# Kernel optimization log

Measured on AMD Instinct MI355X. Metric: run time of the kernel, lower is better.

## Reference

```python
import jax, jax.numpy as jnp
import numpy as np
import math

B, S, HID = 1, 2048, 2048
NH, NKV, HD = 32, 8, 64
GROUPS = NH // NKV
BOOST_SCALE, NARROW_SCALE = 1.0, 4.0
NEG = -1e9


def rope_cos_sin(seq_len, scale):
    inv_freq = 1.0 / (10000.0 ** (jnp.arange(0, HD, 2, dtype=jnp.float32) / HD))
    t = jnp.arange(seq_len, dtype=jnp.float32) / scale
    freqs = jnp.outer(t, inv_freq)                      # [s, hd/2]
    emb = jnp.concatenate([freqs, freqs], axis=-1)      # [s, hd]
    return jnp.cos(emb), jnp.sin(emb)


def rotate_half(x):
    x1, x2 = x[..., : HD // 2], x[..., HD // 2:]
    return jnp.concatenate([-x2, x1], axis=-1)


def apply_rope(q, k, cos, sin, position_ids):
    c = cos[position_ids][:, None]                      # [b,1,s,hd]
    s = sin[position_ids][:, None]
    return q * c + rotate_half(q) * s, k * c + rotate_half(k) * s


def setup_inputs() -> dict:
    key = jax.random.key(0)
    ks = jax.random.split(key, 5)
    hidden_states = jax.random.normal(ks[0], (B, S, HID), dtype=jnp.float32)
    i = jnp.arange(S)[:, None]
    j = jnp.arange(S)[None, :]
    attention_mask = jnp.where(j <= i, 0.0, NEG).astype(jnp.float32)[None, None]  # [1,1,S,S]
    position_ids = jnp.broadcast_to(jnp.arange(S, dtype=jnp.int32)[None], (B, S))
    sc = 1.0 / math.sqrt(HID)
    Wq = jax.random.normal(ks[1], (NH * HD, HID), dtype=jnp.float32) * sc
    Wk = jax.random.normal(ks[2], (NKV * HD, HID), dtype=jnp.float32) * sc
    Wv = jax.random.normal(ks[3], (NKV * HD, HID), dtype=jnp.float32) * sc
    Wo = jax.random.normal(ks[4], (HID, HID), dtype=jnp.float32) * sc
    return dict(hidden_states=hidden_states, attention_mask=attention_mask,
                position_ids=position_ids, Wq=Wq, Wk=Wk, Wv=Wv, Wo=Wo)


def reference(hidden_states, attention_mask, position_ids, Wq, Wk, Wv, Wo):
    b, q_len, _ = hidden_states.shape
    kv_seq_len = q_len

    q = (hidden_states @ Wq.T).reshape(b, q_len, NH, HD).transpose(0, 2, 1, 3)   # [b,H,s,hd]
    k = (hidden_states @ Wk.T).reshape(b, q_len, NKV, HD).transpose(0, 2, 1, 3)  # [b,Hkv,s,hd]
    v = (hidden_states @ Wv.T).reshape(b, q_len, NKV, HD).transpose(0, 2, 1, 3)

    boost_cos, boost_sin = rope_cos_sin(kv_seq_len, BOOST_SCALE)
    narrow_cos, narrow_sin = rope_cos_sin(kv_seq_len + 30, NARROW_SCALE)
    bq, bk = apply_rope(q, k, boost_cos, boost_sin, position_ids)
    nq, nk = apply_rope(q, k, narrow_cos, narrow_sin, position_ids)

    # repeat_kv (GQA)
    bk = jnp.repeat(bk, GROUPS, axis=1)
    nk = jnp.repeat(nk, GROUPS, axis=1)
    v = jnp.repeat(v, GROUPS, axis=1)

    inv_sqrt = 1.0 / math.sqrt(HD)
    big = jnp.einsum('bhqd,bhkd->bhqk', bq, bk) * inv_sqrt
    small = jnp.einsum('bhqd,bhkd->bhqk', nq, nk) * inv_sqrt
    big = big + attention_mask
    small = small + attention_mask

    # neighbor mask: tril minus (for rows >= context_length) tril(diag=context_length)
    # which zeroes those rows entirely -> neighbor = (j <= i) & (i < context_length)
    context_length = q_len - 10
    i = jnp.arange(q_len)[:, None]
    j = jnp.arange(kv_seq_len)[None, :]
    neighbor = (j <= i) & (i < context_length)

    merged = jnp.where(neighbor, big, small)
    probs = jax.nn.softmax(merged.astype(jnp.float32), axis=-1).astype(q.dtype)
    attn = jnp.einsum('bhqk,bhkd->bhqd', probs, v)
    attn = attn.transpose(0, 2, 1, 3).reshape(b, q_len, HID)
    return attn @ Wo.T
```

## Files before the change

kernel.cpp:

```cpp
#include <hip/hip_runtime.h>
#include <math.h>

#define S_LEN 2048
#define HIDN  2048
#define NH    32
#define NKV   8
#define HD    64
#define KVW   (NKV * HD)
#define CTX   (S_LEN - 10)
#define MASKV (-30000.0f)

typedef unsigned short u16;
typedef __attribute__((ext_vector_type(4))) float f32x4;
typedef __attribute__((ext_vector_type(8))) short s16x8;

__device__ __forceinline__ float bf2f(u16 u) {
  union { unsigned int i; float f; } v; v.i = ((unsigned int)u) << 16; return v.f;
}
__device__ __forceinline__ u16 f2bf(float f) {
  union { float f; unsigned int i; } v; v.f = f;
  unsigned int r = v.i + 0x7fffu + ((v.i >> 16) & 1u);
  return (u16)(r >> 16);
}

__global__ __launch_bounds__(256) void conv_all(
    const float* __restrict__ h,  const float* __restrict__ wq,
    const float* __restrict__ wk, const float* __restrict__ wv,
    const float* __restrict__ wo,
    u16* __restrict__ Hb, u16* __restrict__ Wqb, u16* __restrict__ Wkb,
    u16* __restrict__ Wvb, u16* __restrict__ Wob)
{
  const int i = blockIdx.x * 256 + threadIdx.x;
  const float* src; u16* dst; int off;
  if      (i < 1048576) { src = h;  dst = Hb;  off = i; }
  else if (i < 2097152) { src = wq; dst = Wqb; off = i - 1048576; }
  else if (i < 2359296) { src = wk; dst = Wkb; off = i - 2097152; }
  else if (i < 2621440) { src = wv; dst = Wvb; off = i - 2359296; }
  else                  { src = wo; dst = Wob; off = i - 2621440; }
  const float4 f4 = ((const float4*)src)[off];
  ushort4 o4;
  o4.x = f2bf(f4.x); o4.y = f2bf(f4.y); o4.z = f2bf(f4.z); o4.w = f2bf(f4.w);
  ((ushort4*)dst)[off] = o4;
}

#define BM 128
#define BN 128
#define BK 64

template<int OF32>
__device__ __forceinline__ void gemm_body(
    u16* __restrict__ As, u16* __restrict__ Bs,
    const u16* __restrict__ A, const u16* __restrict__ B, void* __restrict__ Cv,
    int N, int K, int row0, int col0, int otrans)
{
  const int tid  = threadIdx.x;
  const int wave = tid >> 6;
  const int lane = tid & 63;
  const int wr = (wave >> 1) * 64;
  const int wc = (wave & 1) * 64;

  f32x4 acc[4][4] = {};

  const int srow = wave * 8 + (lane >> 3);
  const int scol = (lane & 7) * 8;

  for (int kt = 0; kt < K; kt += BK) {
#pragma unroll
    for (int it = 0; it < 4; ++it) {
      const u16* gA = A + (size_t)(row0 + it * 32 + srow) * K + kt + scol;
      const u16* gB = B + (size_t)(col0 + it * 32 + srow) * K + kt + scol;
      u16* lA = &As[(it * 32 + wave * 8) * BK];
      u16* lB = &Bs[(it * 32 + wave * 8) * BK];
      __builtin_amdgcn_global_load_lds((const __attribute__((address_space(1))) void*)gA,
                                       (__attribute__((address_space(3))) void*)lA, 16, 0, 0);
      __builtin_amdgcn_global_load_lds((const __attribute__((address_space(1))) void*)gB,
                                       (__attribute__((address_space(3))) void*)lB, 16, 0, 0);
    }
    __syncthreads();
#pragma unroll
    for (int kk = 0; kk < 2; ++kk) {
      const int ko = kk * 32 + (lane >> 4) * 8;
      s16x8 af[4], bg[4];
#pragma unroll
      for (int mi = 0; mi < 4; ++mi)
        af[mi] = *(const s16x8*)&As[(wr + mi * 16 + (lane & 15)) * BK + ko];
#pragma unroll
      for (int ni = 0; ni < 4; ++ni)
        bg[ni] = *(const s16x8*)&Bs[(wc + ni * 16 + (lane & 15)) * BK + ko];
#pragma unroll
      for (int mi = 0; mi < 4; ++mi)
#pragma unroll
        for (int ni = 0; ni < 4; ++ni)
          acc[mi][ni] = __builtin_amdgcn_mfma_f32_16x16x32_bf16(af[mi], bg[ni], acc[mi][ni], 0, 0, 0);
    }
    __syncthreads();
  }

  const int rq = (lane >> 4) * 4;
  const int cq = lane & 15;
#pragma unroll
  for (int mi = 0; mi < 4; ++mi)
#pragma unroll
    for (int ni = 0; ni < 4; ++ni) {
      const int r = row0 + wr + mi * 16 + rq;
      const int c = col0 + wc + ni * 16 + cq;
      if (otrans) {
        ushort4 o4;
        o4.x = f2bf(acc[mi][ni][0]); o4.y = f2bf(acc[mi][ni][1]);
        o4.z = f2bf(acc[mi][ni][2]); o4.w = f2bf(acc[mi][ni][3]);
        *(ushort4*)&((u16*)Cv)[(size_t)c * S_LEN + r] = o4;
      } else {
#pragma unroll
        for (int t = 0; t < 4; ++t) {
          if (OF32) ((float*)Cv)[(size_t)(r + t) * N + c] = acc[mi][ni][t];
          else      ((u16*)Cv)[(size_t)(r + t) * N + c]   = f2bf(acc[mi][ni][t]);
        }
      }
    }
}

__global__ __launch_bounds__(256) void gemm_qkv(
    const u16* __restrict__ A, const u16* __restrict__ Wq, const u16* __restrict__ Wk,
    const u16* __restrict__ Wv, u16* __restrict__ Q, u16* __restrict__ Kb, u16* __restrict__ Vt)
{
  __shared__ u16 As[BM * BK];
  __shared__ u16 Bs[BN * BK];
  const int bn = blockIdx.x;
  const int row0 = blockIdx.y * BM;
  const u16* Bp; u16* Cp; int N; int col0; int ot;
  if (bn < 16)      { Bp = Wq; Cp = Q;  N = HIDN; col0 = bn * BN;        ot = 0; }
  else if (bn < 20) { Bp = Wk; Cp = Kb; N = KVW;  col0 = (bn - 16) * BN; ot = 0; }
  else              { Bp = Wv; Cp = Vt; N = KVW;  col0 = (bn - 20) * BN; ot = 1; }
  gemm_body<0>(As, Bs, A, Bp, Cp, N, HIDN, row0, col0, ot);
}

__global__ __launch_bounds__(256) void gemm_out(
    const u16* __restrict__ A, const u16* __restrict__ B, float* __restrict__ C, int N, int K)
{
  __shared__ u16 As[BM * BK];
  __shared__ u16 Bs[BN * BK];
  gemm_body<1>(As, Bs, A, B, C, N, K, blockIdx.y * BM, blockIdx.x * BN, 0);
}

__global__ __launch_bounds__(256) void rope_kernel(
    u16* __restrict__ Q, u16* __restrict__ Kb, u16* __restrict__ Kn,
    const int* __restrict__ pos_ids)
{
  const int idx = blockIdx.x * 256 + threadIdx.x;
  const int totq = S_LEN * NH * (HD / 2);
  const float LN1E4 = 9.210340371976184f;
  if (idx < totq) {
    const int d = idx & 31;
    const int h = (idx >> 5) & (NH - 1);
    const int i = idx >> 10;
    const float f = expf(-(float)(2 * d) * (1.0f / HD) * LN1E4);
    const int pos = pos_ids[i];
    const float scl = (i < CTX) ? 1.0f : 0.25f;
    const float ang = ((float)pos * scl) * f;
    const float c = cosf(ang), s = sinf(ang);
    u16* p = Q + (size_t)i * HIDN + h * HD + d;
    const float x1 = bf2f(p[0]), x2 = bf2f(p[32]);
    p[0]  = f2bf((x1 * c - x2 * s) * 0.125f);
    p[32] = f2bf((x2 * c + x1 * s) * 0.125f);
  } else {
    const int k = idx - totq;
    if (k >= S_LEN * NKV * (HD / 2)) return;
    const int d  = k & 31;
    const int kh = (k >> 5) & (NKV - 1);
    const int j  = k >> 8;
    const float f = expf(-(float)(2 * d) * (1.0f / HD) * LN1E4);
    const float pos = (float)pos_ids[j];
    const float cb = cosf(pos * f),          sb = sinf(pos * f);
    const float cn = cosf(pos * 0.25f * f),  sn = sinf(pos * 0.25f * f);
    const size_t off = (size_t)j * KVW + kh * HD + d;
    u16* pb = Kb + off;
    u16* pn = Kn + off;
    const float x1 = bf2f(pb[0]), x2 = bf2f(pb[32]);
    pn[0]  = f2bf(x1 * cn - x2 * sn);
    pn[32] = f2bf(x2 * cn + x1 * sn);
    pb[0]  = f2bf(x1 * cb - x2 * sb);
    pb[32] = f2bf(x2 * cb + x1 * sb);
  }
}

#define PAD 8
__global__ __launch_bounds__(256) void attn_mfma(
    const u16* __restrict__ Q, const u16* __restrict__ K, const u16* __restrict__ Kn,
    const u16* __restrict__ Vt, u16* __restrict__ O)
{
  __shared__ __align__(16) u16 Ks[64][HD + PAD];
  __shared__ __align__(16) u16 Kns[64][HD + PAD];
  __shared__ __align__(16) u16 Vts[HD][64 + PAD];
  __shared__ __align__(16) u16 Ps[4][16][64 + PAD];

  const int tid  = threadIdx.x;
  const int wave = tid >> 6;
  const int lane = tid & 63;
  const int l15  = lane & 15;
  const int quad = lane >> 4;
  const int h    = blockIdx.y;
  const int kh   = h >> 2;
  const int pr   = blockIdx.x;

  int sa[4], sb[4];
#pragma unroll
  for (int it = 0; it < 4; ++it) {
    const int u = it * 256 + tid;
    sa[it] = u >> 4;
    sb[it] = (u & 15) * 4;
  }

  for (int phase = 0; phase < 2; ++phase) {
    const int qt = phase ? pr : 31 - pr;
    const int i_base = qt * 64;
    const int rw0 = i_base + wave * 16;
    const bool mixed_blk = (qt == 31);
    const bool mixed_wv  = mixed_blk && (rw0 + 15 >= CTX);

    s16x8 aq[2];
#pragma unroll
    for (int ks = 0; ks < 2; ++ks)
      aq[ks] = *(const s16x8*)(Q + (size_t)(rw0 + l15) * HIDN + h * HD + ks * 32 + quad * 8);

    f32x4 acc_o[4] = {};
    float l_[4] = {0.f, 0.f, 0.f, 0.f};

    const int ntiles = qt + 1;
    ushort4 kr[4], vr[4], knr[4];
#pragma unroll
    for (int it = 0; it < 4; ++it) {
      kr[it] = *(const ushort4*)(K  + (size_t)(0 + sa[it]) * KVW + kh * HD + sb[it]);
      vr[it] = *(const ushort4*)(Vt + (size_t)(kh * HD + sa[it]) * S_LEN + 0 + sb[it]);
      if (mixed_blk) knr[it] = *(const ushort4*)(Kn + (size_t)(0 + sa[it]) * KVW + kh * HD + sb[it]);
    }

    for (int t = 0; t < ntiles; ++t) {
      const int jt = t * 64;
      __syncthreads();
#pragma unroll
      for (int it = 0; it < 4; ++it) {
        *(ushort4*)&Ks[sa[it]][sb[it]]  = kr[it];
        *(ushort4*)&Vts[sa[it]][sb[it]] = vr[it];
        if (mixed_blk) *(ushort4*)&Kns[sa[it]][sb[it]] = knr[it];
      }
      __syncthreads();
      if (t + 1 < ntiles) {
        const int jn = jt + 64;
#pragma unroll
        for (int it = 0; it < 4; ++it) {
          kr[it] = *(const ushort4*)(K  + (size_t)(jn + sa[it]) * KVW + kh * HD + sb[it]);
          vr[it] = *(const ushort4*)(Vt + (size_t)(kh * HD + sa[it]) * S_LEN + jn + sb[it]);
          if (mixed_blk) knr[it] = *(const ushort4*)(Kn + (size_t)(jn + sa[it]) * KVW + kh * HD + sb[it]);
        }
      }

      f32x4 sc4[4] = {};
#pragma unroll
      for (int ks = 0; ks < 2; ++ks) {
        const int ko = ks * 32 + quad * 8;
#pragma unroll
        for (int nb = 0; nb < 4; ++nb) {
          const s16x8 bk = *(const s16x8*)&Ks[nb * 16 + l15][ko];
          sc4[nb] = __builtin_amdgcn_mfma_f32_16x16x32_bf16(aq[ks], bk, sc4[nb], 0, 0, 0);
        }
      }
      if (mixed_wv) {
        f32x4 sc4n[4] = {};
#pragma unroll
        for (int ks = 0; ks < 2; ++ks) {
          const int ko = ks * 32 + quad * 8;
#pragma unroll
          for (int nb = 0; nb < 4; ++nb) {
            const s16x8 bk = *(const s16x8*)&Kns[nb * 16 + l15][ko];
            sc4n[nb] = __builtin_amdgcn_mfma_f32_16x16x32_bf16(aq[ks], bk, sc4n[nb], 0, 0, 0);
          }
        }
#pragma unroll
        for (int reg = 0; reg < 4; ++reg) {
          const bool narrow = (rw0 + quad * 4 + reg >= CTX);
#pragma unroll
          for (int nb = 0; nb < 4; ++nb)
            sc4[nb][reg] = narrow ? sc4n[nb][reg] : sc4[nb][reg];
        }
      }

      const int lr0 = quad * 4;
#pragma unroll
      for (int reg = 0; reg < 4; ++reg) {
        const int rowg = rw0 + lr0 + reg;
#pragma unroll
        for (int nb = 0; nb < 4; ++nb) {
          float p = __expf(fminf(sc4[nb][reg], 60.f));
          p = (jt + nb * 16 + l15 > rowg) ? 0.f : p;
          l_[reg] += p;
          Ps[wave][lr0 + reg][nb * 16 + l15] = f2bf(p);
        }
      }
      __threadfence_block();

#pragma unroll
      for (int ks = 0; ks < 2; ++ks) {
        const int ko = ks * 32 + quad * 8;
        const s16x8 ap = *(const s16x8*)&Ps[wave][l15][ko];
#pragma unroll
        for (int nb = 0; nb < 4; ++nb) {
          const s16x8 bv = *(const s16x8*)&Vts[nb * 16 + l15][ko];
          acc_o[nb] = __builtin_amdgcn_mfma_f32_16x16x32_bf16(ap, bv, acc_o[nb], 0, 0, 0);
        }
      }
    }

    const int lr0 = quad * 4;
#pragma unroll
    for (int reg = 0; reg < 4; ++reg) {
      float s = l_[reg];
      s += __shfl_xor(s, 1, 64);
      s += __shfl_xor(s, 2, 64);
      s += __shfl_xor(s, 4, 64);
      s += __shfl_xor(s, 8, 64);
      const float inv = 1.0f / fmaxf(s, 1e-30f);
      const int rowg = rw0 + lr0 + reg;
#pragma unroll
      for (int nb = 0; nb < 4; ++nb)
        O[(size_t)rowg * HIDN + h * HD + nb * 16 + l15] = f2bf(acc_o[nb][reg] * inv);
    }
  }
}

extern "C" void kernel_launch(void* const* d_in, const int* in_sizes, int n_in,
                              void* d_out, int out_size, void* d_ws, size_t ws_size,
                              hipStream_t stream)
{
  const float* hidden = (const float*)d_in[0];
  const int* pos      = (const int*)d_in[2];
  const float* Wq = (const float*)d_in[3];
  const float* Wk = (const float*)d_in[4];
  const float* Wv = (const float*)d_in[5];
  const float* Wo = (const float*)d_in[6];
  float* out = (float*)d_out;

  char* ws = (char*)d_ws;
  u16* Qb  = (u16*)(ws);
  u16* Kbb = (u16*)(ws + (8u  << 20));
  u16* Knb = (u16*)(ws + (10u << 20));
  u16* Vtb = (u16*)(ws + (12u << 20));
  u16* Ab  = (u16*)(ws + (14u << 20));
  u16* Hb  = (u16*)(ws + (22u << 20));
  u16* Wqb = (u16*)(ws + (30u << 20));
  u16* Wkb = (u16*)(ws + (38u << 20));
  u16* Wvb = (u16*)(ws + (40u << 20));
  u16* Wob = (u16*)(ws + (42u << 20));

  conv_all<<<dim3(14336), 256, 0, stream>>>(hidden, Wq, Wk, Wv, Wo, Hb, Wqb, Wkb, Wvb, Wob);
  gemm_qkv<<<dim3(24, 16), 256, 0, stream>>>(Hb, Wqb, Wkb, Wvb, Qb, Kbb, Vtb);
  const int tot = S_LEN * NH * (HD / 2) + S_LEN * NKV * (HD / 2);
  rope_kernel<<<dim3((tot + 255) / 256), 256, 0, stream>>>(Qb, Kbb, Knb, pos);
  attn_mfma<<<dim3(16, NH), 256, 0, stream>>>(Qb, Kbb, Knb, Vtb, Ab);
  gemm_out<<<dim3(16, 16), 256, 0, stream>>>(Ab, Wob, out, HIDN, HIDN);
}
```

Measured before the change: 281.3 us.

## Rewrite attention with 32x32 MFMA, register-resident P via permlane swap, exp2 scaling

Restructures the attention kernel to use 32x32x16 bf16 MFMA with each wave owning 32 query rows and a 128-row block. S is computed transposed so that P stays in registers: it is packed with v_cvt_pk_bf16 and rearranged with v_permlane32_swap, which removes the LDS round-trip for P. The log2(e) factor is folded into the Q scaling so the kernel can call exp2 directly, and causal masking only runs on diagonal tiles. The trade-offs are that the causal workload is no longer paired across blocks, which worsens load balance, and that the kernel now uses larger accumulators and more registers.

```diff
diff --git a/kernel.cpp b/kernel.cpp
--- a/kernel.cpp
+++ b/kernel.cpp
@@ -8,10 +8,10 @@
 #define HD    64
 #define KVW   (NKV * HD)
 #define CTX   (S_LEN - 10)
-#define MASKV (-30000.0f)
 
 typedef unsigned short u16;
 typedef __attribute__((ext_vector_type(4))) float f32x4;
+typedef __attribute__((ext_vector_type(16))) float f32x16;
 typedef __attribute__((ext_vector_type(8))) short s16x8;
 
 __device__ __forceinline__ float bf2f(u16 u) {
@@ -21,6 +21,11 @@
   union { float f; unsigned int i; } v; v.f = f;
   unsigned int r = v.i + 0x7fffu + ((v.i >> 16) & 1u);
   return (u16)(r >> 16);
+}
+__device__ __forceinline__ unsigned int cvt_pk_bf16(float a, float b) {
+  unsigned int d;
+  asm("v_cvt_pk_bf16_f32 %0, %1, %2" : "=v"(d) : "v"(a), "v"(b));
+  return d;
 }
 
 __global__ __launch_bounds__(256) void conv_all(
@@ -149,6 +154,7 @@
   const int idx = blockIdx.x * 256 + threadIdx.x;
   const int totq = S_LEN * NH * (HD / 2);
   const float LN1E4 = 9.210340371976184f;
+  const float QSCL  = 0.18033688011112042f;
   if (idx < totq) {
     const int d = idx & 31;
     const int h = (idx >> 5) & (NH - 1);
@@ -160,8 +166,8 @@
     const float c = cosf(ang), s = sinf(ang);
     u16* p = Q + (size_t)i * HIDN + h * HD + d;
     const float x1 = bf2f(p[0]), x2 = bf2f(p[32]);
-    p[0]  = f2bf((x1 * c - x2 * s) * 0.125f);
-    p[32] = f2bf((x2 * c + x1 * s) * 0.125f);
+    p[0]  = f2bf((x1 * c - x2 * s) * QSCL);
+    p[32] = f2bf((x2 * c + x1 * s) * QSCL);
   } else {
     const int k = idx - totq;
     if (k >= S_LEN * NKV * (HD / 2)) return;
@@ -191,139 +197,135 @@
   __shared__ __align__(16) u16 Ks[64][HD + PAD];
   __shared__ __align__(16) u16 Kns[64][HD + PAD];
   __shared__ __align__(16) u16 Vts[HD][64 + PAD];
-  __shared__ __align__(16) u16 Ps[4][16][64 + PAD];
+  __shared__ float l_sh[4][32];
 
   const int tid  = threadIdx.x;
   const int wave = tid >> 6;
   const int lane = tid & 63;
-  const int l15  = lane & 15;
-  const int quad = lane >> 4;
+  const int l31  = lane & 31;
+  const int hi   = lane >> 5;
   const int h    = blockIdx.y;
   const int kh   = h >> 2;
-  const int pr   = blockIdx.x;
-
-  int sa[4], sb[4];
-#pragma unroll
-  for (int it = 0; it < 4; ++it) {
+  const int qb   = 15 - (int)blockIdx.x;
+  const int rw0  = qb * 128 + wave * 32;
+  const bool mixed_blk = (qb == 15);
+  const bool mixed_wv  = mixed_blk && (rw0 + 31 >= CTX);
+
+  int sa[2], sb[2];
+#pragma unroll
+  for (int it = 0; it < 2; ++it) {
     const int u = it * 256 + tid;
-    sa[it] = u >> 4;
-    sb[it] = (u & 15) * 4;
-  }
-
-  for (int phase = 0; phase < 2; ++phase) {
-    const int qt = phase ? pr : 31 - pr;
-    const int i_base = qt * 64;
-    const int rw0 = i_base + wave * 16;
-    const bool mixed_blk = (qt == 31);
-    const bool mixed_wv  = mixed_blk && (rw0 + 15 >= CTX);
-
-    s16x8 aq[2];
-#pragma unroll
-    for (int ks = 0; ks < 2; ++ks)
-      aq[ks] = *(const s16x8*)(Q + (size_t)(rw0 + l15) * HIDN + h * HD + ks * 32 + quad * 8);
-
-    f32x4 acc_o[4] = {};
-    float l_[4] = {0.f, 0.f, 0.f, 0.f};
-
-    const int ntiles = qt + 1;
-    ushort4 kr[4], vr[4], knr[4];
-#pragma unroll
-    for (int it = 0; it < 4; ++it) {
-      kr[it] = *(const ushort4*)(K  + (size_t)(0 + sa[it]) * KVW + kh * HD + sb[it]);
-      vr[it] = *(const ushort4*)(Vt + (size_t)(kh * HD + sa[it]) * S_LEN + 0 + sb[it]);
-      if (mixed_blk) knr[it] = *(const ushort4*)(Kn + (size_t)(0 + sa[it]) * KVW + kh * HD + sb[it]);
-    }
-
-    for (int t = 0; t < ntiles; ++t) {
-      const int jt = t * 64;
-      __syncthreads();
-#pragma unroll
-      for (int it = 0; it < 4; ++it) {
-        *(ushort4*)&Ks[sa[it]][sb[it]]  = kr[it];
-        *(ushort4*)&Vts[sa[it]][sb[it]] = vr[it];
-        if (mixed_blk) *(ushort4*)&Kns[sa[it]][sb[it]] = knr[it];
-      }
-      __syncthreads();
-      if (t + 1 < ntiles) {
-        const int jn = jt + 64;
-#pragma unroll
-        for (int it = 0; it < 4; ++it) {
-          kr[it] = *(const ushort4*)(K  + (size_t)(jn + sa[it]) * KVW + kh * HD + sb[it]);
-          vr[it] = *(const ushort4*)(Vt + (size_t)(kh * HD + sa[it]) * S_LEN + jn + sb[it]);
-          if (mixed_blk) knr[it] = *(const ushort4*)(Kn + (size_t)(jn + sa[it]) * KVW + kh * HD + sb[it]);
+    sa[it] = u >> 3;
+    sb[it] = (u & 7) * 8;
+  }
+
+  s16x8 bq[4];
+#pragma unroll
+  for (int i = 0; i < 4; ++i)
+    bq[i] = *(const s16x8*)(Q + (size_t)(rw0 + l31) * HIDN + h * HD + i * 16 + hi * 8);
+
+  f32x16 acc0 = {};
+  f32x16 acc1 = {};
+  float lsum = 0.f;
+
+  const int ntiles = 2 * qb + 2;
+  s16x8 kr[2], vr[2], knr[2];
+#pragma unroll
+  for (int it = 0; it < 2; ++it) {
+    kr[it] = *(const s16x8*)(K  + (size_t)sa[it] * KVW + kh * HD + sb[it]);
+    vr[it] = *(const s16x8*)(Vt + (size_t)(kh * HD + sa[it]) * S_LEN + sb[it]);
+    if (mixed_blk) knr[it] = *(const s16x8*)(Kn + (size_t)sa[it] * KVW + kh * HD + sb[it]);
+  }
+
+  for (int t = 0; t < ntiles; ++t) {
+    const int jt = t * 64;
+    __syncthreads();
+#pragma unroll
+    for (int it = 0; it < 2; ++it) {
+      *(s16x8*)&Ks[sa[it]][sb[it]]  = kr[it];
+      *(s16x8*)&Vts[sa[it]][sb[it]] = vr[it];
+      if (mixed_blk) *(s16x8*)&Kns[sa[it]][sb[it]] = knr[it];
+    }
+    __syncthreads();
+    if (t + 1 < ntiles) {
+      const int jn = jt + 64;
+#pragma unroll
+      for (int it = 0; it < 2; ++it) {
+        kr[it] = *(const s16x8*)(K  + (size_t)(jn + sa[it]) * KVW + kh * HD + sb[it]);
+        vr[it] = *(const s16x8*)(Vt + (size_t)(kh * HD + sa[it]) * S_LEN + jn + sb[it]);
+        if (mixed_blk) knr[it] = *(const s16x8*)(Kn + (size_t)(jn + sa[it]) * KVW + kh * HD + sb[it]);
+      }
+    }
+
+    if (jt > rw0 + 31) continue;
+    const bool needmask = (jt + 63 > rw0);
+
+#pragma unroll
+    for (int g = 0; g < 2; ++g) {
+      f32x16 sc = {};
+#pragma unroll
+      for (int i = 0; i < 4; ++i) {
+        const s16x8 ak = *(const s16x8*)&Ks[g * 32 + l31][i * 16 + hi * 8];
+        sc = __builtin_amdgcn_mfma_f32_32x32x16_bf16(ak, bq[i], sc, 0, 0, 0);
+      }
+      if (mixed_wv) {
+        f32x16 scn = {};
+#pragma unroll
+        for (int i = 0; i < 4; ++i) {
+          const s16x8 ak = *(const s16x8*)&Kns[g * 32 + l31][i * 16 + hi * 8];
+          scn = __builtin_amdgcn_mfma_f32_32x32x16_bf16(ak, bq[i], scn, 0, 0, 0);
         }
-      }
-
-      f32x4 sc4[4] = {};
-#pragma unroll
-      for (int ks = 0; ks < 2; ++ks) {
-        const int ko = ks * 32 + quad * 8;
-#pragma unroll
-        for (int nb = 0; nb < 4; ++nb) {
-          const s16x8 bk = *(const s16x8*)&Ks[nb * 16 + l15][ko];
-          sc4[nb] = __builtin_amdgcn_mfma_f32_16x16x32_bf16(aq[ks], bk, sc4[nb], 0, 0, 0);
+        const bool nar = (rw0 + l31) >= CTX;
+#pragma unroll
+        for (int r = 0; r < 16; ++r) sc[r] = nar ? scn[r] : sc[r];
+      }
+
+      float p[16];
+#pragma unroll
+      for (int r = 0; r < 16; ++r) {
+        float e = __builtin_amdgcn_exp2f(fminf(sc[r], 80.f));
+        if (needmask) {
+          const int key = jt + g * 32 + (r & 3) + 8 * (r >> 2) + 4 * hi;
+          e = (key > rw0 + l31) ? 0.f : e;
         }
-      }
-      if (mixed_wv) {
-        f32x4 sc4n[4] = {};
-#pragma unroll
-        for (int ks = 0; ks < 2; ++ks) {
-          const int ko = ks * 32 + quad * 8;
-#pragma unroll
-          for (int nb = 0; nb < 4; ++nb) {
-            const s16x8 bk = *(const s16x8*)&Kns[nb * 16 + l15][ko];
-            sc4n[nb] = __builtin_amdgcn_mfma_f32_16x16x32_bf16(aq[ks], bk, sc4n[nb], 0, 0, 0);
-          }
-        }
-#pragma unroll
-        for (int reg = 0; reg < 4; ++reg) {
-          const bool narrow = (rw0 + quad * 4 + reg >= CTX);
-#pragma unroll
-          for (int nb = 0; nb < 4; ++nb)
-            sc4[nb][reg] = narrow ? sc4n[nb][reg] : sc4[nb][reg];
-        }
-      }
-
-      const int lr0 = quad * 4;
-#pragma unroll
-      for (int reg = 0; reg < 4; ++reg) {
-        const int rowg = rw0 + lr0 + reg;
-#pragma unroll
-        for (int nb = 0; nb < 4; ++nb) {
-          float p = __expf(fminf(sc4[nb][reg], 60.f));
-          p = (jt + nb * 16 + l15 > rowg) ? 0.f : p;
-          l_[reg] += p;
-          Ps[wave][lr0 + reg][nb * 16 + l15] = f2bf(p);
-        }
-      }
-      __threadfence_block();
-
-#pragma unroll
-      for (int ks = 0; ks < 2; ++ks) {
-        const int ko = ks * 32 + quad * 8;
-        const s16x8 ap = *(const s16x8*)&Ps[wave][l15][ko];
-#pragma unroll
-        for (int nb = 0; nb < 4; ++nb) {
-          const s16x8 bv = *(const s16x8*)&Vts[nb * 16 + l15][ko];
-          acc_o[nb] = __builtin_amdgcn_mfma_f32_16x16x32_bf16(ap, bv, acc_o[nb], 0, 0, 0);
-        }
-      }
-    }
-
-    const int lr0 = quad * 4;
-#pragma unroll
-    for (int reg = 0; reg < 4; ++reg) {
-      float s = l_[reg];
-      s += __shfl_xor(s, 1, 64);
-      s += __shfl_xor(s, 2, 64);
-      s += __shfl_xor(s, 4, 64);
-      s += __shfl_xor(s, 8, 64);
-      const float inv = 1.0f / fmaxf(s, 1e-30f);
-      const int rowg = rw0 + lr0 + reg;
-#pragma unroll
-      for (int nb = 0; nb < 4; ++nb)
-        O[(size_t)rowg * HIDN + h * HD + nb * 16 + l15] = f2bf(acc_o[nb][reg] * inv);
-    }
+        p[r] = e;
+        lsum += e;
+      }
+
+      unsigned int c[4][2];
+#pragma unroll
+      for (int blk = 0; blk < 4; ++blk) {
+        c[blk][0] = cvt_pk_bf16(p[4 * blk + 0], p[4 * blk + 1]);
+        c[blk][1] = cvt_pk_bf16(p[4 * blk + 2], p[4 * blk + 3]);
+      }
+
+#pragma unroll
+      for (int s = 0; s < 2; ++s) {
+        unsigned int w0 = c[2 * s][0], w2 = c[2 * s + 1][0];
+        unsigned int w1 = c[2 * s][1], w3 = c[2 * s + 1][1];
+        asm("v_permlane32_swap_b32 %0, %1" : "+v"(w0), "+v"(w2));
+        asm("v_permlane32_swap_b32 %0, %1" : "+v"(w1), "+v"(w3));
+        union { unsigned int u[4]; s16x8 v; } af;
+        af.u[0] = w0; af.u[1] = w1; af.u[2] = w2; af.u[3] = w3;
+        const int kc = g * 32 + s * 16 + hi * 8;
+        const s16x8 v0 = *(const s16x8*)&Vts[l31][kc];
+        const s16x8 v1 = *(const s16x8*)&Vts[32 + l31][kc];
+        acc0 = __builtin_amdgcn_mfma_f32_32x32x16_bf16(af.v, v0, acc0, 0, 0, 0);
+        acc1 = __builtin_amdgcn_mfma_f32_32x32x16_bf16(af.v, v1, acc1, 0, 0, 0);
+      }
+    }
+  }
+
+  lsum += __shfl_xor(lsum, 32, 64);
+  const float inv = 1.0f / fmaxf(lsum, 1e-30f);
+  if (hi == 0) l_sh[wave][l31] = inv;
+#pragma unroll
+  for (int r = 0; r < 16; ++r) {
+    const int rl = (r & 3) + 8 * (r >> 2) + 4 * hi;
+    const float iv = l_sh[wave][rl];
+    const size_t o = (size_t)(rw0 + rl) * HIDN + h * HD + l31;
+    O[o]      = f2bf(acc0[r] * iv);
+    O[o + 32] = f2bf(acc1[r] * iv);
   }
 }
 
```

New measurement: 296.8 us. 5.5% more time.
